# Kernel optimization log

Measured on AMD Instinct MI355X. Metric: run time of the kernel, lower is better.

## Reference

```python
import jax, jax.numpy as jnp
import numpy as np

N = 100_000      # nodes
E = 3_200_000    # edges (avg degree 32)
F_IN = 37        # NCI1 num_features
H = 16           # hidden
C = 2            # NCI1 num_classes


def setup_inputs() -> dict:
    key = jax.random.key(0)
    k = jax.random.split(key, 7)
    x = jax.random.normal(k[0], (N, F_IN), dtype=jnp.float32)
    edge_index = jax.random.randint(k[1], (2, E), 0, N, dtype=jnp.int32)
    edge_weight = jax.random.uniform(k[2], (E,), dtype=jnp.float32)
    # Glorot-ish init for the two GCN linear weights, zero bias (PyG default)
    W1 = jax.random.normal(k[3], (F_IN, H), dtype=jnp.float32) * (1.0 / np.sqrt(F_IN))
    b1 = jnp.zeros((H,), dtype=jnp.float32)
    W2 = jax.random.normal(k[4], (H, C), dtype=jnp.float32) * (1.0 / np.sqrt(H))
    b2 = jnp.zeros((C,), dtype=jnp.float32)
    return {"x": x, "edge_index": edge_index, "edge_weight": edge_weight,
            "W1": W1, "b1": b1, "W2": W2, "b2": b2}


def _gcn_norm(edge_index, edge_weight, dtype):
    # PyG gcn_norm: add self-loops (weight 1.0), symmetric D^-1/2 A D^-1/2
    loop = jnp.arange(N, dtype=edge_index.dtype)
    row = jnp.concatenate([edge_index[0], loop])  # source
    col = jnp.concatenate([edge_index[1], loop])  # target (aggregation index)
    w = jnp.concatenate([edge_weight, jnp.ones((N,), dtype=dtype)])
    deg = jax.ops.segment_sum(w, col, num_segments=N)
    dinv = jnp.where(deg > 0, jax.lax.rsqrt(deg), 0.0).astype(dtype)
    norm = dinv[row] * w * dinv[col]  # [E+N]
    return row, col, norm


def _gcn_layer(x, row, col, norm, W, b):
    h = x @ W                                   # small dense transform first
    msg = norm[:, None] * h[row]                # gather + scale, [E+N, out]
    out = jax.ops.segment_sum(msg, col, num_segments=N)  # scatter-add
    return out + b


def reference(x, edge_index, edge_weight, W1, b1, W2, b2):
    row, col, norm = _gcn_norm(edge_index, edge_weight, x.dtype)
    h = jax.nn.relu(_gcn_layer(x, row, col, norm, W1, b1))
    # F.dropout with training=False is identity (module evaluated in eval mode)
    h = _gcn_layer(h, row, col, norm, W2, b2)
    return jax.nn.log_softmax(h, axis=1)
```

## Files before the change

### kernel.cpp

```cpp
#include <hip/hip_runtime.h>
#include <math.h>

#define N_NODES 100000
#define N_EDGES 3200000
#define F_IN    37
#define H_DIM   16
#define C_DIM   2

#define BUCKET_BITS 7
#define BUCKET_SZ   128
#define NBUCK       782
#define CAP         4736
#define CHUNK       16384
#define NCHUNK      196
#define EPT         16
#define EPT_S       5

__device__ __forceinline__ unsigned bf16rne(float f) {
    unsigned u = __float_as_uint(f);
    return (u + 0x7FFFu + ((u >> 16) & 1u)) >> 16;
}
__device__ __forceinline__ int2 ldnt_i2(const int2* p) {
    long long v = __builtin_nontemporal_load((const long long*)p);
    return *(int2*)&v;
}
#define BLO(u) __uint_as_float((u) << 16)
#define BHI(u) __uint_as_float((u) & 0xFFFF0000u)
#define EW(u)  __uint_as_float(((u) >> 17) << 16)
#define ER(u)  ((u) & 0x1FFFFu)

__global__ void k_init(int* __restrict__ gcur) {
    int i = blockIdx.x * blockDim.x + threadIdx.x;
    if (i < NBUCK) gcur[i] = i * CAP;
}

__global__ __launch_bounds__(1024) void k_part(
    const int* __restrict__ row, const int* __restrict__ col,
    const float* __restrict__ w, int* __restrict__ gcur, int2* __restrict__ ebuf)
{
    __shared__ int cnt[NBUCK];
    __shared__ int gbase[NBUCK];
    int t = threadIdx.x;
    int e0 = blockIdx.x * CHUNK;
    int bk[EPT], rc[EPT], lofs[EPT];
    float wv[EPT];

    if (t < NBUCK) cnt[t] = 0;
    __syncthreads();
#pragma unroll
    for (int k = 0; k < EPT; k++) {
        int e = e0 + k * 1024 + t;
        if (e < N_EDGES) {
            int r = __builtin_nontemporal_load(&row[e]);
            int c = __builtin_nontemporal_load(&col[e]);
            wv[k] = __builtin_nontemporal_load(&w[e]);
            bk[k] = c >> BUCKET_BITS;
            rc[k] = r | ((c & (BUCKET_SZ - 1)) << 17);
            lofs[k] = atomicAdd(&cnt[bk[k]], 1);
        } else bk[k] = -1;
    }
    __syncthreads();
    if (t < NBUCK) gbase[t] = atomicAdd(&gcur[t], cnt[t]);
    __syncthreads();
#pragma unroll
    for (int k = 0; k < EPT; k++) {
        if (bk[k] >= 0)
            ebuf[gbase[bk[k]] + lofs[k]] = make_int2(rc[k], __float_as_int(wv[k]));
    }
}

__global__ __launch_bounds__(1024) void k_sort(
    const int* __restrict__ gcur, const int2* __restrict__ ebuf,
    unsigned* __restrict__ ebuf4, int2* __restrict__ rp, float* __restrict__ dinv)
{
    __shared__ int  cnt[BUCKET_SZ];
    __shared__ int  base[BUCKET_SZ];
    __shared__ int2 stage[CAP];
    int t = threadIdx.x, b = blockIdx.x;
    int s = b * CAP;
    int len = gcur[b] - s;
    if (t < BUCKET_SZ) cnt[t] = 0;
    __syncthreads();

    int2 ed[EPT_S]; int cl[EPT_S], lofs[EPT_S];
#pragma unroll
    for (int k = 0; k < EPT_S; k++) {
        int i = k * 1024 + t;
        if (i < len) {
            int2 v = ldnt_i2(&ebuf[s + i]);
            ed[k] = v;
            cl[k] = v.x >> 17;
            lofs[k] = atomicAdd(&cnt[cl[k]], 1);
        } else cl[k] = -1;
    }
    __syncthreads();
    if (t < BUCKET_SZ) base[t] = cnt[t];
    __syncthreads();
    for (int off = 1; off < BUCKET_SZ; off <<= 1) {
        int v2 = 0;
        if (t < BUCKET_SZ && t >= off) v2 = base[t - off];
        __syncthreads();
        if (t < BUCKET_SZ) base[t] += v2;
        __syncthreads();
    }
#pragma unroll
    for (int k = 0; k < EPT_S; k++) {
        if (cl[k] >= 0) {
            int pos = base[cl[k]] - cnt[cl[k]] + lofs[k];
            stage[pos] = ed[k];
        }
    }
    __syncthreads();
    for (int i = t; i < len; i += 1024) {
        int2 v = stage[i];
        unsigned wb = bf16rne(__int_as_float(v.y));
        ebuf4[s + i] = (wb << 17) | (unsigned)(v.x & 0x1FFFF);
    }
    if (t < BUCKET_SZ) {
        int c = (b << BUCKET_BITS) + t;
        if (c < N_NODES) {
            int st = base[t] - cnt[t], n = cnt[t];
            float sum = 1.0f;
            for (int i = 0; i < n; i++) sum += __int_as_float(stage[st + i].y);
            rp[c] = make_int2(s + st, n);
            dinv[c] = rsqrtf(sum);
        }
    }
}

__global__ __launch_bounds__(256) void k_xw1(
    const float* __restrict__ x, const float* __restrict__ W1,
    const float* __restrict__ dinv, uint4* __restrict__ h1b)
{
    __shared__ float xs[256 * F_IN];
    __shared__ float sW[F_IN * H_DIM];
    int t = threadIdx.x;
    int nb = blockIdx.x * 256;
    for (int idx = t; idx < F_IN * H_DIM; idx += 256) sW[idx] = W1[idx];
    int g0 = nb * F_IN;
    for (int idx = t; idx < 256 * F_IN; idx += 256) {
        int gi = g0 + idx;
        if (gi < N_NODES * F_IN) xs[idx] = __builtin_nontemporal_load(&x[gi]);
    }
    __syncthreads();
    int i = nb + t;
    if (i >= N_NODES) return;
    float acc[H_DIM];
#pragma unroll
    for (int j = 0; j < H_DIM; j++) acc[j] = 0.f;
    const float* xi = &xs[t * F_IN];
    for (int k = 0; k < F_IN; k++) {
        float xv = xi[k];
#pragma unroll
        for (int j = 0; j < H_DIM; j++) acc[j] += xv * sW[k * H_DIM + j];
    }
    float di = dinv[i];
    unsigned p[8];
#pragma unroll
    for (int j = 0; j < 8; j++) {
        unsigned lo = bf16rne(di * acc[2 * j]);
        unsigned hi = bf16rne(di * acc[2 * j + 1]);
        p[j] = lo | (hi << 16);
    }
    h1b[(size_t)i * 2 + 0] = make_uint4(p[0], p[1], p[2], p[3]);
    h1b[(size_t)i * 2 + 1] = make_uint4(p[4], p[5], p[6], p[7]);
}

__global__ __launch_bounds__(256) void k_agg1(
    const int2* __restrict__ rp, const unsigned* __restrict__ ebuf4,
    const uint2* __restrict__ h1b, const float* __restrict__ dinv,
    const float* __restrict__ b1, const float* __restrict__ W2,
    float* __restrict__ h2s)
{
    __shared__ float sW2[H_DIM * C_DIM];
    __shared__ float sb1[H_DIM];
    int t = threadIdx.x;
    if (t < H_DIM * C_DIM) sW2[t] = W2[t];
    if (t >= 32 && t < 32 + H_DIM) sb1[t - 32] = b1[t - 32];
    __syncthreads();
    int id = blockIdx.x * 256 + t;
    int c = id >> 3;
    int sub = id & 7, q = sub & 3, h = sub >> 2;
    if (c >= N_NODES) return;
    int2 seg = rp[c];
    int s = seg.x, n = seg.y;
    int m = (n - h + 1) >> 1;
    int p0i = s + h;
    float4 acc = make_float4(0.f, 0.f, 0.f, 0.f);

#define PROC1(u)                                                    \
    {   float a = EW(u);                                            \
        uint2 g = h1b[(size_t)ER(u) * 4 + q];                       \
        acc.x += a * BLO(g.x); acc.y += a * BHI(g.x);               \
        acc.z += a * BLO(g.y); acc.w += a * BHI(g.y); }

    int k = 0;
    if (m >= 4) {
        unsigned e0 = __builtin_nontemporal_load(&ebuf4[p0i + 0]);
        unsigned e1 = __builtin_nontemporal_load(&ebuf4[p0i + 2]);
        unsigned e2 = __builtin_nontemporal_load(&ebuf4[p0i + 4]);
        unsigned e3 = __builtin_nontemporal_load(&ebuf4[p0i + 6]);
        for (; k + 8 <= m; k += 4) {
            unsigned f0 = __builtin_nontemporal_load(&ebuf4[p0i + 2 * (k + 4)]);
            unsigned f1 = __builtin_nontemporal_load(&ebuf4[p0i + 2 * (k + 5)]);
            unsigned f2 = __builtin_nontemporal_load(&ebuf4[p0i + 2 * (k + 6)]);
            unsigned f3 = __builtin_nontemporal_load(&ebuf4[p0i + 2 * (k + 7)]);
            PROC1(e0); PROC1(e1); PROC1(e2); PROC1(e3);
            e0 = f0; e1 = f1; e2 = f2; e3 = f3;
        }
        PROC1(e0); PROC1(e1); PROC1(e2); PROC1(e3);
        k += 4;
    }
    for (; k < m; k++) {
        unsigned u = __builtin_nontemporal_load(&ebuf4[p0i + 2 * k]);
        PROC1(u);
    }
#undef PROC1

    acc.x += __shfl_xor(acc.x, 4);
    acc.y += __shfl_xor(acc.y, 4);
    acc.z += __shfl_xor(acc.z, 4);
    acc.w += __shfl_xor(acc.w, 4);

    float dc = dinv[c];
    uint2 gc = h1b[(size_t)c * 4 + q];
    float hcv[4] = {BLO(gc.x), BHI(gc.x), BLO(gc.y), BHI(gc.y)};
    float av[4] = {acc.x + hcv[0], acc.y + hcv[1], acc.z + hcv[2], acc.w + hcv[3]};
    int j0 = q << 2;
    float p0 = 0.f, p1 = 0.f;
#pragma unroll
    for (int j = 0; j < 4; j++) {
        float rv = fmaxf(dc * av[j] + sb1[j0 + j], 0.f);
        p0 += rv * sW2[(j0 + j) * C_DIM + 0];
        p1 += rv * sW2[(j0 + j) * C_DIM + 1];
    }
    p0 += __shfl_xor(p0, 1); p0 += __shfl_xor(p0, 2);
    p1 += __shfl_xor(p1, 1); p1 += __shfl_xor(p1, 2);
    if (sub == 0) ((float2*)h2s)[c] = make_float2(dc * p0, dc * p1);
}

__global__ __launch_bounds__(256) void k_agg2(
    const int2* __restrict__ rp, const unsigned* __restrict__ ebuf4,
    const float* __restrict__ h2s, const float* __restrict__ dinv,
    const float* __restrict__ b2, float* __restrict__ out)
{
    int id = blockIdx.x * 256 + threadIdx.x;
    int c = id >> 2, sub = id & 3;
    if (c >= N_NODES) return;
    int2 seg = rp[c];
    int s = seg.x, n = seg.y;
    const float2* h22 = (const float2*)h2s;
    int m = (n - sub + 3) >> 2;
    int p0i = s + sub;
    float a0 = 0.f, a1 = 0.f;

#define PROC2(u)                                                    \
    {   float a = EW(u);                                            \
        float2 hv = h22[ER(u)];                                     \
        a0 += a * hv.x;  a1 += a * hv.y; }

    int k = 0;
    if (m >= 4) {
        unsigned e0 = __builtin_nontemporal_load(&ebuf4[p0i + 0]);
        unsigned e1 = __builtin_nontemporal_load(&ebuf4[p0i + 4]);
        unsigned e2 = __builtin_nontemporal_load(&ebuf4[p0i + 8]);
        unsigned e3 = __builtin_nontemporal_load(&ebuf4[p0i + 12]);
        for (; k + 8 <= m; k += 4) {
            unsigned f0 = __builtin_nontemporal_load(&ebuf4[p0i + 4 * (k + 4)]);
            unsigned f1 = __builtin_nontemporal_load(&ebuf4[p0i + 4 * (k + 5)]);
            unsigned f2 = __builtin_nontemporal_load(&ebuf4[p0i + 4 * (k + 6)]);
            unsigned f3 = __builtin_nontemporal_load(&ebuf4[p0i + 4 * (k + 7)]);
            PROC2(e0); PROC2(e1); PROC2(e2); PROC2(e3);
            e0 = f0; e1 = f1; e2 = f2; e3 = f3;
        }
        PROC2(e0); PROC2(e1); PROC2(e2); PROC2(e3);
        k += 4;
    }
    for (; k < m; k++) {
        unsigned u = __builtin_nontemporal_load(&ebuf4[p0i + 4 * k]);
        PROC2(u);
    }
#undef PROC2

    a0 += __shfl_xor(a0, 1); a0 += __shfl_xor(a0, 2);
    a1 += __shfl_xor(a1, 1); a1 += __shfl_xor(a1, 2);
    if (sub == 0) {
        float dc = dinv[c];
        float2 hc = h22[c];
        float l0 = dc * (a0 + hc.x) + b2[0];
        float l1 = dc * (a1 + hc.y) + b2[1];
        float mx = fmaxf(l0, l1);
        float lse = mx + logf(expf(l0 - mx) + expf(l1 - mx));
        ((float2*)out)[c] = make_float2(l0 - lse, l1 - lse);
    }
}

extern "C" void kernel_launch(void* const* d_in, const int* in_sizes, int n_in,
                              void* d_out, int out_size, void* d_ws, size_t ws_size,
                              hipStream_t stream) {
    const float* x  = (const float*)d_in[0];
    const int*   ei = (const int*)d_in[1];
    const float* w  = (const float*)d_in[2];
    const float* W1 = (const float*)d_in[3];
    const float* b1 = (const float*)d_in[4];
    const float* W2 = (const float*)d_in[5];
    const float* b2 = (const float*)d_in[6];
    float* out = (float*)d_out;

    const int* row = ei;
    const int* col = ei + N_EDGES;

    char* ws = (char*)d_ws;
    int*      gcur  = (int*)(ws + 0);
    int2*     rp    = (int2*)(ws + 3200);
    float*    dinv  = (float*)(ws + 803200);
    uint4*    h1b   = (uint4*)(ws + 1203200);
    float*    h2s   = (float*)(ws + 4403200);
    unsigned* ebuf4 = (unsigned*)(ws + 5203200);
    int2*     ebuf  = (int2*)(ws + 20017408);

    k_init <<<4, 256, 0, stream>>>(gcur);
    k_part <<<NCHUNK, 1024, 0, stream>>>(row, col, w, gcur, ebuf);
    k_sort <<<NBUCK, 1024, 0, stream>>>(gcur, ebuf, ebuf4, rp, dinv);
    k_xw1  <<<(N_NODES + 255) / 256, 256, 0, stream>>>(x, W1, dinv, h1b);
    k_agg1 <<<(8 * N_NODES + 255) / 256, 256, 0, stream>>>(rp, ebuf4, (const uint2*)h1b, dinv, b1, W2, h2s);
    k_agg2 <<<(4 * N_NODES + 255) / 256, 256, 0, stream>>>(rp, ebuf4, h2s, dinv, b2, out);
}
```

Before: 222.7 us.

## Fuse bucket sort with layer-1 aggregation and compute degrees via global atomics

Degree accumulation moves into the partition kernel as global float atomicAdds on deg, so dinv is recomputed as rsqrt(deg+1) wherever it is needed. That removes the dependency on the sort kernel and lets x@W1 run before the sort. The sort kernel is merged with layer-1 aggregation: each bucket block reads its sorted edges directly from shared memory with fp32 weights, so the ebuf4 reload for layer 1 is gone. The trade-offs are 3.2M global float atomics with a nondeterministic summation order, and an aggregation phase of only 128 nodes × 8 threads per 1024-thread block, which can leave threads idle and lower occupancy.

```diff
diff --git a/kernel.cpp b/kernel.cpp
--- a/kernel.cpp
+++ b/kernel.cpp
@@ -29,14 +29,16 @@
 #define EW(u)  __uint_as_float(((u) >> 17) << 16)
 #define ER(u)  ((u) & 0x1FFFFu)
 
-__global__ void k_init(int* __restrict__ gcur) {
+__global__ void k_init(int* __restrict__ gcur, float* __restrict__ deg) {
     int i = blockIdx.x * blockDim.x + threadIdx.x;
     if (i < NBUCK) gcur[i] = i * CAP;
+    if (i < N_NODES) deg[i] = 0.f;
 }
 
 __global__ __launch_bounds__(1024) void k_part(
     const int* __restrict__ row, const int* __restrict__ col,
-    const float* __restrict__ w, int* __restrict__ gcur, int2* __restrict__ ebuf)
+    const float* __restrict__ w, int* __restrict__ gcur,
+    int2* __restrict__ ebuf, float* __restrict__ deg)
 {
     __shared__ int cnt[NBUCK];
     __shared__ int gbase[NBUCK];
@@ -57,6 +59,7 @@
             bk[k] = c >> BUCKET_BITS;
             rc[k] = r | ((c & (BUCKET_SZ - 1)) << 17);
             lofs[k] = atomicAdd(&cnt[bk[k]], 1);
+            atomicAdd(&deg[c], wv[k]);
         } else bk[k] = -1;
     }
     __syncthreads();
@@ -69,68 +72,9 @@
     }
 }
 
-__global__ __launch_bounds__(1024) void k_sort(
-    const int* __restrict__ gcur, const int2* __restrict__ ebuf,
-    unsigned* __restrict__ ebuf4, int2* __restrict__ rp, float* __restrict__ dinv)
-{
-    __shared__ int  cnt[BUCKET_SZ];
-    __shared__ int  base[BUCKET_SZ];
-    __shared__ int2 stage[CAP];
-    int t = threadIdx.x, b = blockIdx.x;
-    int s = b * CAP;
-    int len = gcur[b] - s;
-    if (t < BUCKET_SZ) cnt[t] = 0;
-    __syncthreads();
-
-    int2 ed[EPT_S]; int cl[EPT_S], lofs[EPT_S];
-#pragma unroll
-    for (int k = 0; k < EPT_S; k++) {
-        int i = k * 1024 + t;
-        if (i < len) {
-            int2 v = ldnt_i2(&ebuf[s + i]);
-            ed[k] = v;
-            cl[k] = v.x >> 17;
-            lofs[k] = atomicAdd(&cnt[cl[k]], 1);
-        } else cl[k] = -1;
-    }
-    __syncthreads();
-    if (t < BUCKET_SZ) base[t] = cnt[t];
-    __syncthreads();
-    for (int off = 1; off < BUCKET_SZ; off <<= 1) {
-        int v2 = 0;
-        if (t < BUCKET_SZ && t >= off) v2 = base[t - off];
-        __syncthreads();
-        if (t < BUCKET_SZ) base[t] += v2;
-        __syncthreads();
-    }
-#pragma unroll
-    for (int k = 0; k < EPT_S; k++) {
-        if (cl[k] >= 0) {
-            int pos = base[cl[k]] - cnt[cl[k]] + lofs[k];
-            stage[pos] = ed[k];
-        }
-    }
-    __syncthreads();
-    for (int i = t; i < len; i += 1024) {
-        int2 v = stage[i];
-        unsigned wb = bf16rne(__int_as_float(v.y));
-        ebuf4[s + i] = (wb << 17) | (unsigned)(v.x & 0x1FFFF);
-    }
-    if (t < BUCKET_SZ) {
-        int c = (b << BUCKET_BITS) + t;
-        if (c < N_NODES) {
-            int st = base[t] - cnt[t], n = cnt[t];
-            float sum = 1.0f;
-            for (int i = 0; i < n; i++) sum += __int_as_float(stage[st + i].y);
-            rp[c] = make_int2(s + st, n);
-            dinv[c] = rsqrtf(sum);
-        }
-    }
-}
-
 __global__ __launch_bounds__(256) void k_xw1(
     const float* __restrict__ x, const float* __restrict__ W1,
-    const float* __restrict__ dinv, uint4* __restrict__ h1b)
+    const float* __restrict__ deg, uint4* __restrict__ h1b)
 {
     __shared__ float xs[256 * F_IN];
     __shared__ float sW[F_IN * H_DIM];
@@ -154,7 +98,7 @@
 #pragma unroll
         for (int j = 0; j < H_DIM; j++) acc[j] += xv * sW[k * H_DIM + j];
     }
-    float di = dinv[i];
+    float di = rsqrtf(deg[i] + 1.0f);
     unsigned p[8];
 #pragma unroll
     for (int j = 0; j < 8; j++) {
@@ -166,55 +110,90 @@
     h1b[(size_t)i * 2 + 1] = make_uint4(p[4], p[5], p[6], p[7]);
 }
 
-__global__ __launch_bounds__(256) void k_agg1(
-    const int2* __restrict__ rp, const unsigned* __restrict__ ebuf4,
-    const uint2* __restrict__ h1b, const float* __restrict__ dinv,
+__global__ __launch_bounds__(1024) void k_sortagg1(
+    const int* __restrict__ gcur, const int2* __restrict__ ebuf,
+    const uint2* __restrict__ h1b, const float* __restrict__ deg,
     const float* __restrict__ b1, const float* __restrict__ W2,
+    unsigned* __restrict__ ebuf4, int2* __restrict__ rp,
     float* __restrict__ h2s)
 {
+    __shared__ int2  stage[CAP];
+    __shared__ int   cnt[BUCKET_SZ];
+    __shared__ int   base[BUCKET_SZ];
     __shared__ float sW2[H_DIM * C_DIM];
     __shared__ float sb1[H_DIM];
-    int t = threadIdx.x;
-    if (t < H_DIM * C_DIM) sW2[t] = W2[t];
-    if (t >= 32 && t < 32 + H_DIM) sb1[t - 32] = b1[t - 32];
-    __syncthreads();
-    int id = blockIdx.x * 256 + t;
-    int c = id >> 3;
-    int sub = id & 7, q = sub & 3, h = sub >> 2;
+    int t = threadIdx.x, b = blockIdx.x;
+    int s = b * CAP;
+    int len = gcur[b] - s;
+    int nbase = b << BUCKET_BITS;
+    if (t < BUCKET_SZ) cnt[t] = 0;
+    if (t >= 256 && t < 256 + H_DIM * C_DIM) sW2[t - 256] = W2[t - 256];
+    if (t >= 512 && t < 512 + H_DIM) sb1[t - 512] = b1[t - 512];
+    __syncthreads();
+
+    int2 ed[EPT_S]; int cl[EPT_S], lofs[EPT_S];
+#pragma unroll
+    for (int k = 0; k < EPT_S; k++) {
+        int i = k * 1024 + t;
+        if (i < len) {
+            int2 v = ldnt_i2(&ebuf[s + i]);
+            ed[k] = v;
+            cl[k] = v.x >> 17;
+            lofs[k] = atomicAdd(&cnt[cl[k]], 1);
+        } else cl[k] = -1;
+    }
+    __syncthreads();
+    if (t < BUCKET_SZ) base[t] = cnt[t];
+    __syncthreads();
+    for (int off = 1; off < BUCKET_SZ; off <<= 1) {
+        int v2 = 0;
+        if (t < BUCKET_SZ && t >= off) v2 = base[t - off];
+        __syncthreads();
+        if (t < BUCKET_SZ) base[t] += v2;
+        __syncthreads();
+    }
+#pragma unroll
+    for (int k = 0; k < EPT_S; k++) {
+        if (cl[k] >= 0) {
+            int pos = base[cl[k]] - cnt[cl[k]] + lofs[k];
+            stage[pos] = ed[k];
+        }
+    }
+    __syncthreads();
+
+    for (int i = t; i < len; i += 1024) {
+        int2 v = stage[i];
+        unsigned wb = bf16rne(__int_as_float(v.y));
+        ebuf4[s + i] = (wb << 17) | (unsigned)(v.x & 0x1FFFF);
+    }
+    if (t < BUCKET_SZ) {
+        int c = nbase + t;
+        if (c < N_NODES) rp[c] = make_int2(s + base[t] - cnt[t], cnt[t]);
+    }
+
+    int n = t >> 3, sub = t & 7, q = sub & 3, h = sub >> 2;
+    int c = nbase + n;
     if (c >= N_NODES) return;
-    int2 seg = rp[c];
-    int s = seg.x, n = seg.y;
-    int m = (n - h + 1) >> 1;
-    int p0i = s + h;
+    int st = base[n] - cnt[n], cn = cnt[n];
+    int m = (cn - h + 1) >> 1;
+    int idx = st + h;
     float4 acc = make_float4(0.f, 0.f, 0.f, 0.f);
 
-#define PROC1(u)                                                    \
-    {   float a = EW(u);                                            \
-        uint2 g = h1b[(size_t)ER(u) * 4 + q];                       \
+#define PROC1(v)                                                    \
+    {   float a = __int_as_float((v).y);                            \
+        uint2 g = h1b[(size_t)((v).x & 0x1FFFF) * 4 + q];           \
         acc.x += a * BLO(g.x); acc.y += a * BHI(g.x);               \
         acc.z += a * BLO(g.y); acc.w += a * BHI(g.y); }
 
     int k = 0;
-    if (m >= 4) {
-        unsigned e0 = __builtin_nontemporal_load(&ebuf4[p0i + 0]);
-        unsigned e1 = __builtin_nontemporal_load(&ebuf4[p0i + 2]);
-        unsigned e2 = __builtin_nontemporal_load(&ebuf4[p0i + 4]);
-        unsigned e3 = __builtin_nontemporal_load(&ebuf4[p0i + 6]);
-        for (; k + 8 <= m; k += 4) {
-            unsigned f0 = __builtin_nontemporal_load(&ebuf4[p0i + 2 * (k + 4)]);
-            unsigned f1 = __builtin_nontemporal_load(&ebuf4[p0i + 2 * (k + 5)]);
-            unsigned f2 = __builtin_nontemporal_load(&ebuf4[p0i + 2 * (k + 6)]);
-            unsigned f3 = __builtin_nontemporal_load(&ebuf4[p0i + 2 * (k + 7)]);
-            PROC1(e0); PROC1(e1); PROC1(e2); PROC1(e3);
-            e0 = f0; e1 = f1; e2 = f2; e3 = f3;
-        }
-        PROC1(e0); PROC1(e1); PROC1(e2); PROC1(e3);
-        k += 4;
-    }
-    for (; k < m; k++) {
-        unsigned u = __builtin_nontemporal_load(&ebuf4[p0i + 2 * k]);
-        PROC1(u);
-    }
+    for (; k + 4 <= m; k += 4) {
+        int2 u0 = stage[idx + 2 * k];
+        int2 u1 = stage[idx + 2 * (k + 1)];
+        int2 u2 = stage[idx + 2 * (k + 2)];
+        int2 u3 = stage[idx + 2 * (k + 3)];
+        PROC1(u0); PROC1(u1); PROC1(u2); PROC1(u3);
+    }
+    for (; k < m; k++) { int2 u = stage[idx + 2 * k]; PROC1(u); }
 #undef PROC1
 
     acc.x += __shfl_xor(acc.x, 4);
@@ -222,7 +201,7 @@
     acc.z += __shfl_xor(acc.z, 4);
     acc.w += __shfl_xor(acc.w, 4);
 
-    float dc = dinv[c];
+    float dc = rsqrtf(deg[c] + 1.0f);
     uint2 gc = h1b[(size_t)c * 4 + q];
     float hcv[4] = {BLO(gc.x), BHI(gc.x), BLO(gc.y), BHI(gc.y)};
     float av[4] = {acc.x + hcv[0], acc.y + hcv[1], acc.z + hcv[2], acc.w + hcv[3]};
@@ -241,7 +220,7 @@
 
 __global__ __launch_bounds__(256) void k_agg2(
     const int2* __restrict__ rp, const unsigned* __restrict__ ebuf4,
-    const float* __restrict__ h2s, const float* __restrict__ dinv,
+    const float* __restrict__ h2s, const float* __restrict__ deg,
     const float* __restrict__ b2, float* __restrict__ out)
 {
     int id = blockIdx.x * 256 + threadIdx.x;
@@ -285,7 +264,7 @@
     a0 += __shfl_xor(a0, 1); a0 += __shfl_xor(a0, 2);
     a1 += __shfl_xor(a1, 1); a1 += __shfl_xor(a1, 2);
     if (sub == 0) {
-        float dc = dinv[c];
+        float dc = rsqrtf(deg[c] + 1.0f);
         float2 hc = h22[c];
         float l0 = dc * (a0 + hc.x) + b2[0];
         float l1 = dc * (a1 + hc.y) + b2[1];
@@ -313,16 +292,16 @@
     char* ws = (char*)d_ws;
     int*      gcur  = (int*)(ws + 0);
     int2*     rp    = (int2*)(ws + 3200);
-    float*    dinv  = (float*)(ws + 803200);
+    float*    deg   = (float*)(ws + 803200);
     uint4*    h1b   = (uint4*)(ws + 1203200);
     float*    h2s   = (float*)(ws + 4403200);
     unsigned* ebuf4 = (unsigned*)(ws + 5203200);
     int2*     ebuf  = (int2*)(ws + 20017408);
 
-    k_init <<<4, 256, 0, stream>>>(gcur);
-    k_part <<<NCHUNK, 1024, 0, stream>>>(row, col, w, gcur, ebuf);
-    k_sort <<<NBUCK, 1024, 0, stream>>>(gcur, ebuf, ebuf4, rp, dinv);
-    k_xw1  <<<(N_NODES + 255) / 256, 256, 0, stream>>>(x, W1, dinv, h1b);
-    k_agg1 <<<(8 * N_NODES + 255) / 256, 256, 0, stream>>>(rp, ebuf4, (const uint2*)h1b, dinv, b1, W2, h2s);
-    k_agg2 <<<(4 * N_NODES + 255) / 256, 256, 0, stream>>>(rp, ebuf4, h2s, dinv, b2, out);
-}
+    k_init    <<<391, 256, 0, stream>>>(gcur, deg);
+    k_part    <<<NCHUNK, 1024, 0, stream>>>(row, col, w, gcur, ebuf, deg);
+    k_xw1     <<<(N_NODES + 255) / 256, 256, 0, stream>>>(x, W1, deg, h1b);
+    k_sortagg1<<<NBUCK, 1024, 0, stream>>>(gcur, ebuf, (const uint2*)h1b, deg,
+                                           b1, W2, ebuf4, rp, h2s);
+    k_agg2    <<<(4 * N_NODES + 255) / 256, 256, 0, stream>>>(rp, ebuf4, h2s, deg, b2, out);
+}
```

Result: slower. 364.9 us (+63.9%).

## Fuse X·W1 transform into bucket sort kernel and use nontemporal stores

Applied to the files above, without the earlier changes.

Merges the dense X·W1 kernel into the per-bucket sort kernel, so each 128-node bucket computes its degree normalisation and then its transformed features, reusing the shared staging buffer for x rows. This removes one launch and the global round trip for dinv before scaling. The matmul now uses 8 threads per node, each producing two outputs, instead of one thread per node. Partition and sort writes switch to nontemporal stores. The cost is more shared-memory and register pressure in an already heavy 1024-thread kernel, and extra serial work appended to the sort phase.

```diff
diff --git a/kernel.cpp b/kernel.cpp
--- a/kernel.cpp
+++ b/kernel.cpp
@@ -23,6 +23,9 @@
 __device__ __forceinline__ int2 ldnt_i2(const int2* p) {
     long long v = __builtin_nontemporal_load((const long long*)p);
     return *(int2*)&v;
+}
+__device__ __forceinline__ void stnt_i2(int2* p, int2 v) {
+    __builtin_nontemporal_store(*(long long*)&v, (long long*)p);
 }
 #define BLO(u) __uint_as_float((u) << 16)
 #define BHI(u) __uint_as_float((u) & 0xFFFF0000u)
@@ -65,20 +68,28 @@
 #pragma unroll
     for (int k = 0; k < EPT; k++) {
         if (bk[k] >= 0)
-            ebuf[gbase[bk[k]] + lofs[k]] = make_int2(rc[k], __float_as_int(wv[k]));
-    }
-}
-
-__global__ __launch_bounds__(1024) void k_sort(
+            stnt_i2(&ebuf[gbase[bk[k]] + lofs[k]],
+                    make_int2(rc[k], __float_as_int(wv[k])));
+    }
+}
+
+__global__ __launch_bounds__(1024) void k_sortxw1(
     const int* __restrict__ gcur, const int2* __restrict__ ebuf,
-    unsigned* __restrict__ ebuf4, int2* __restrict__ rp, float* __restrict__ dinv)
+    const float* __restrict__ x, const float* __restrict__ W1,
+    unsigned* __restrict__ ebuf4, int2* __restrict__ rp,
+    float* __restrict__ dinv, unsigned* __restrict__ h1b)
 {
-    __shared__ int  cnt[BUCKET_SZ];
-    __shared__ int  base[BUCKET_SZ];
-    __shared__ int2 stage[CAP];
+    __shared__ int2  stage[CAP];
+    __shared__ int   cnt[BUCKET_SZ];
+    __shared__ int   base[BUCKET_SZ];
+    __shared__ float sdinv[BUCKET_SZ];
+    __shared__ float sW[F_IN * H_DIM];
+    float* xs = (float*)stage;
+
     int t = threadIdx.x, b = blockIdx.x;
     int s = b * CAP;
     int len = gcur[b] - s;
+    int nbase = b << BUCKET_BITS;
     if (t < BUCKET_SZ) cnt[t] = 0;
     __syncthreads();
 
@@ -114,56 +125,47 @@
     for (int i = t; i < len; i += 1024) {
         int2 v = stage[i];
         unsigned wb = bf16rne(__int_as_float(v.y));
-        ebuf4[s + i] = (wb << 17) | (unsigned)(v.x & 0x1FFFF);
+        __builtin_nontemporal_store((wb << 17) | (unsigned)(v.x & 0x1FFFF),
+                                    &ebuf4[s + i]);
     }
     if (t < BUCKET_SZ) {
-        int c = (b << BUCKET_BITS) + t;
+        int c = nbase + t;
+        int st = base[t] - cnt[t], n = cnt[t];
+        float sum = 1.0f;
+        for (int i = 0; i < n; i++) sum += __int_as_float(stage[st + i].y);
+        float di = rsqrtf(sum);
+        sdinv[t] = di;
         if (c < N_NODES) {
-            int st = base[t] - cnt[t], n = cnt[t];
-            float sum = 1.0f;
-            for (int i = 0; i < n; i++) sum += __int_as_float(stage[st + i].y);
             rp[c] = make_int2(s + st, n);
-            dinv[c] = rsqrtf(sum);
-        }
-    }
-}
-
-__global__ __launch_bounds__(256) void k_xw1(
-    const float* __restrict__ x, const float* __restrict__ W1,
-    const float* __restrict__ dinv, uint4* __restrict__ h1b)
-{
-    __shared__ float xs[256 * F_IN];
-    __shared__ float sW[F_IN * H_DIM];
-    int t = threadIdx.x;
-    int nb = blockIdx.x * 256;
-    for (int idx = t; idx < F_IN * H_DIM; idx += 256) sW[idx] = W1[idx];
-    int g0 = nb * F_IN;
-    for (int idx = t; idx < 256 * F_IN; idx += 256) {
+            dinv[c] = di;
+        }
+    }
+    __syncthreads();
+
+    for (int idx = t; idx < F_IN * H_DIM; idx += 1024) sW[idx] = W1[idx];
+    int g0 = nbase * F_IN;
+    int nfl = BUCKET_SZ * F_IN;
+    for (int idx = t; idx < nfl; idx += 1024) {
         int gi = g0 + idx;
-        if (gi < N_NODES * F_IN) xs[idx] = __builtin_nontemporal_load(&x[gi]);
-    }
-    __syncthreads();
-    int i = nb + t;
-    if (i >= N_NODES) return;
-    float acc[H_DIM];
-#pragma unroll
-    for (int j = 0; j < H_DIM; j++) acc[j] = 0.f;
-    const float* xi = &xs[t * F_IN];
-    for (int k = 0; k < F_IN; k++) {
-        float xv = xi[k];
-#pragma unroll
-        for (int j = 0; j < H_DIM; j++) acc[j] += xv * sW[k * H_DIM + j];
-    }
-    float di = dinv[i];
-    unsigned p[8];
-#pragma unroll
-    for (int j = 0; j < 8; j++) {
-        unsigned lo = bf16rne(di * acc[2 * j]);
-        unsigned hi = bf16rne(di * acc[2 * j + 1]);
-        p[j] = lo | (hi << 16);
-    }
-    h1b[(size_t)i * 2 + 0] = make_uint4(p[0], p[1], p[2], p[3]);
-    h1b[(size_t)i * 2 + 1] = make_uint4(p[4], p[5], p[6], p[7]);
+        xs[idx] = (gi < N_NODES * F_IN) ? __builtin_nontemporal_load(&x[gi]) : 0.f;
+    }
+    __syncthreads();
+    {
+        int n = t >> 3, sub = t & 7;
+        int c = nbase + n;
+        if (c < N_NODES) {
+            const float* xi = &xs[n * F_IN];
+            float a0 = 0.f, a1 = 0.f;
+            for (int k = 0; k < F_IN; k++) {
+                float xv = xi[k];
+                a0 += xv * sW[k * H_DIM + 2 * sub];
+                a1 += xv * sW[k * H_DIM + 2 * sub + 1];
+            }
+            float di = sdinv[n];
+            unsigned pk = bf16rne(di * a0) | (bf16rne(di * a1) << 16);
+            h1b[(size_t)c * 8 + sub] = pk;
+        }
+    }
 }
 
 __global__ __launch_bounds__(256) void k_agg1(
@@ -314,15 +316,14 @@
     int*      gcur  = (int*)(ws + 0);
     int2*     rp    = (int2*)(ws + 3200);
     float*    dinv  = (float*)(ws + 803200);
-    uint4*    h1b   = (uint4*)(ws + 1203200);
+    unsigned* h1b   = (unsigned*)(ws + 1203200);
     float*    h2s   = (float*)(ws + 4403200);
     unsigned* ebuf4 = (unsigned*)(ws + 5203200);
     int2*     ebuf  = (int2*)(ws + 20017408);
 
-    k_init <<<4, 256, 0, stream>>>(gcur);
-    k_part <<<NCHUNK, 1024, 0, stream>>>(row, col, w, gcur, ebuf);
-    k_sort <<<NBUCK, 1024, 0, stream>>>(gcur, ebuf, ebuf4, rp, dinv);
-    k_xw1  <<<(N_NODES + 255) / 256, 256, 0, stream>>>(x, W1, dinv, h1b);
-    k_agg1 <<<(8 * N_NODES + 255) / 256, 256, 0, stream>>>(rp, ebuf4, (const uint2*)h1b, dinv, b1, W2, h2s);
-    k_agg2 <<<(4 * N_NODES + 255) / 256, 256, 0, stream>>>(rp, ebuf4, h2s, dinv, b2, out);
-}
+    k_init    <<<4, 256, 0, stream>>>(gcur);
+    k_part    <<<NCHUNK, 1024, 0, stream>>>(row, col, w, gcur, ebuf);
+    k_sortxw1 <<<NBUCK, 1024, 0, stream>>>(gcur, ebuf, x, W1, ebuf4, rp, dinv, h1b);
+    k_agg1    <<<(8 * N_NODES + 255) / 256, 256, 0, stream>>>(rp, ebuf4, (const uint2*)h1b, dinv, b1, W2, h2s);
+    k_agg2    <<<(4 * N_NODES + 255) / 256, 256, 0, stream>>>(rp, ebuf4, h2s, dinv, b2, out);
+}
```

New measurement: 299.8 us. 1.35x slower.
